# Kernel optimization log

Measured on AMD Instinct MI355X. Metric: run time of the kernel, lower is better.

The kernel has to match this reference:

```python
import jax, jax.numpy as jnp
import numpy as np

H, T, D = 16, 4096, 64   # heads, total packed tokens, head_dim
NSEQ = 8                 # packed variable-length sequences

def setup_inputs() -> dict:
    key = jax.random.key(0)
    k1, k2, k3 = jax.random.split(key, 3)
    q = jax.random.normal(k1, (1, H, T, D), dtype=jnp.float32)
    k = jax.random.normal(k2, (1, H, T, D), dtype=jnp.float32)
    v = jax.random.normal(k3, (1, H, T, D), dtype=jnp.float32)
    # cu_seqlens: prefix sums of per-sequence lengths (equal 512-token segments here)
    cu_seqlens = jnp.arange(NSEQ + 1, dtype=jnp.int32) * (T // NSEQ)
    return {"q": q, "k": k, "v": v, "cu_seqlens": cu_seqlens,
            "block_q_len": 128, "block_k_len": 512}

def reference(q, k, v, cu_seqlens, block_q_len, block_k_len):
    # Faithful to source: scale = 1.0 / d**(-0.5) == sqrt(d)
    d = q.shape[-1]
    scale = 1.0 / d ** (-0.5)
    # [1,H,T,D] -> [T,H,D] packed layout (transpose(1,2).squeeze(0))
    qp = jnp.swapaxes(q, 1, 2)[0]
    kp = jnp.swapaxes(k, 1, 2)[0]
    vp = jnp.swapaxes(v, 1, 2)[0]
    t = qp.shape[0]
    # segment id of each packed token from cu_seqlens
    seg = jnp.searchsorted(cu_seqlens[1:], jnp.arange(t), side="right")
    # tokens attend only within their own sequence (causal=False, dropout=0)
    mask = seg[:, None] == seg[None, :]                      # [T,T]
    scores = jnp.einsum("qhd,khd->hqk", qp, kp) * scale      # [H,T,T]
    scores = jnp.where(mask[None, :, :], scores, -jnp.inf)
    p = jax.nn.softmax(scores, axis=-1)
    out = jnp.einsum("hqk,khd->qhd", p, vp)                  # [T,H,D]
    return out
```

## Files before the change

kernel.cpp:

```cpp
#include <hip/hip_runtime.h>
#include <stdint.h>

typedef float  f32x4  __attribute__((ext_vector_type(4)));
typedef short  bf16x8 __attribute__((ext_vector_type(8)));
typedef unsigned short u16;
typedef u16    u16x4  __attribute__((ext_vector_type(4)));

#define HD 16
#define DD 64
#define BQ 64
#define BK 64

__device__ __forceinline__ u16 f2bf(float f) {
  uint32_t u = __float_as_uint(f);
  u = (u + 0x7FFFu + ((u >> 16) & 1u)) >> 16;
  return (u16)u;
}

__device__ __forceinline__ bf16x8 ldsw8(const u16* base, int row, int col) {
  int idx = (row * 64 + col) ^ ((row & 7) << 3);
  return *reinterpret_cast<const bf16x8*>(base + idx);
}

__global__ __launch_bounds__(256) void fa_fwd(
    const float* __restrict__ q, const float* __restrict__ k,
    const float* __restrict__ v, const int* __restrict__ cu,
    float* __restrict__ out, int T, int nseq)
{
  __shared__ __align__(16) u16 sKhi[BK * DD];
  __shared__ __align__(16) u16 sKlo[BK * DD];
  __shared__ __align__(16) u16 sVt [DD * BK];
  __shared__ __align__(16) u16 sP  [4][16 * BK];

  const int tile = blockIdx.x;
  const int h    = blockIdx.y;

  int seg = -1, row0 = 0, sbeg = 0, send = 0;
  {
    int acc = 0;
    for (int s = 0; s < nseq; ++s) {
      int b = cu[s], e = cu[s + 1];
      int nt = (e - b + BQ - 1) >> 6;
      if (seg < 0 && tile < acc + nt) {
        seg = s;
        int local = tile - acc;
        row0 = b + local * BQ; sbeg = b; send = e;
      }
      acc += nt;
    }
  }
  if (seg < 0) return;
  const int rows = min(BQ, send - row0);

  const int tid  = threadIdx.x;
  const int wv   = tid >> 6;
  const int lane = tid & 63;
  const int g    = lane >> 4;
  const int c    = lane & 15;

  const float SC = 8.0f * 1.4426950408889634f;
  bf16x8 qhi[2], qlo[2];
  {
    const int  qrl = wv * 16 + c;
    const bool qok = qrl < rows;
    const float* qp = q + ((size_t)h * T + (row0 + qrl)) * DD;
    for (int w = 0; w < 2; ++w) {
      int d0 = w * 32 + g * 8;
      float f[8];
      if (qok) {
        float4 a = *reinterpret_cast<const float4*>(qp + d0);
        float4 b = *reinterpret_cast<const float4*>(qp + d0 + 4);
        f[0]=a.x; f[1]=a.y; f[2]=a.z; f[3]=a.w;
        f[4]=b.x; f[5]=b.y; f[6]=b.z; f[7]=b.w;
      } else {
        for (int i = 0; i < 8; ++i) f[i] = 0.f;
      }
      for (int i = 0; i < 8; ++i) {
        float s  = f[i] * SC;
        u16   hb = f2bf(s);
        float hf = __uint_as_float(((uint32_t)hb) << 16);
        u16   lb = f2bf(s - hf);
        qhi[w][i] = (short)hb;
        qlo[w][i] = (short)lb;
      }
    }
  }

  f32x4 zero4 = {0.f, 0.f, 0.f, 0.f};
  f32x4 oacc[4];
  for (int dt = 0; dt < 4; ++dt) oacc[dt] = zero4;
  float mrun[4], lrun[4];
  for (int j = 0; j < 4; ++j) { mrun[j] = -1e30f; lrun[j] = 0.f; }

  for (int kt0 = sbeg; kt0 < send; kt0 += BK) {
    for (int p = 0; p < 4; ++p) {
      int key = p * 16 + (tid >> 4);
      int d0  = (tid & 15) * 4;
      int gk  = kt0 + key;
      float4 kv = {0,0,0,0}, vv = {0,0,0,0};
      if (gk < send) {
        kv = *reinterpret_cast<const float4*>(k + ((size_t)h * T + gk) * DD + d0);
        vv = *reinterpret_cast<const float4*>(v + ((size_t)h * T + gk) * DD + d0);
      }
      float kf[4] = {kv.x, kv.y, kv.z, kv.w};
      u16x4 hi4, lo4;
      for (int i = 0; i < 4; ++i) {
        u16   hb = f2bf(kf[i]);
        float hf = __uint_as_float(((uint32_t)hb) << 16);
        hi4[i] = hb;
        lo4[i] = f2bf(kf[i] - hf);
      }
      int kidx = (key * 64 + d0) ^ ((key & 7) << 3);
      *reinterpret_cast<u16x4*>(sKhi + kidx) = hi4;
      *reinterpret_cast<u16x4*>(sKlo + kidx) = lo4;
      float vf[4] = {vv.x, vv.y, vv.z, vv.w};
      for (int i = 0; i < 4; ++i) {
        int d = d0 + i;
        sVt[(d * 64 + key) ^ ((d & 7) << 3)] = f2bf(vf[i]);
      }
    }
    __syncthreads();

    f32x4 sacc[4];
    for (int kt = 0; kt < 4; ++kt) sacc[kt] = zero4;
    for (int kt = 0; kt < 4; ++kt) {
      int krow = kt * 16 + c;
      bf16x8 kh0 = ldsw8(sKhi, krow,      g * 8);
      bf16x8 kh1 = ldsw8(sKhi, krow, 32 + g * 8);
      bf16x8 kl0 = ldsw8(sKlo, krow,      g * 8);
      bf16x8 kl1 = ldsw8(sKlo, krow, 32 + g * 8);
      sacc[kt] = __builtin_amdgcn_mfma_f32_16x16x32_bf16(qhi[0], kh0, sacc[kt], 0, 0, 0);
      sacc[kt] = __builtin_amdgcn_mfma_f32_16x16x32_bf16(qhi[1], kh1, sacc[kt], 0, 0, 0);
      sacc[kt] = __builtin_amdgcn_mfma_f32_16x16x32_bf16(qlo[0], kh0, sacc[kt], 0, 0, 0);
      sacc[kt] = __builtin_amdgcn_mfma_f32_16x16x32_bf16(qlo[1], kh1, sacc[kt], 0, 0, 0);
      sacc[kt] = __builtin_amdgcn_mfma_f32_16x16x32_bf16(qhi[0], kl0, sacc[kt], 0, 0, 0);
      sacc[kt] = __builtin_amdgcn_mfma_f32_16x16x32_bf16(qhi[1], kl1, sacc[kt], 0, 0, 0);
    }

    if (kt0 + BK > send) {
      for (int kt = 0; kt < 4; ++kt) {
        int gk = kt0 + kt * 16 + c;
        if (gk >= send) {
          sacc[kt][0] = -3.0e38f; sacc[kt][1] = -3.0e38f;
          sacc[kt][2] = -3.0e38f; sacc[kt][3] = -3.0e38f;
        }
      }
    }

    float mrow[4];
    for (int j = 0; j < 4; ++j)
      mrow[j] = fmaxf(fmaxf(sacc[0][j], sacc[1][j]), fmaxf(sacc[2][j], sacc[3][j]));
    for (int off = 1; off < 16; off <<= 1)
      for (int j = 0; j < 4; ++j)
        mrow[j] = fmaxf(mrow[j], __shfl_xor(mrow[j], off, 64));

    float alpha[4];
    for (int j = 0; j < 4; ++j) {
      float mn = fmaxf(mrun[j], mrow[j]);
      alpha[j] = exp2f(mrun[j] - mn);
      mrun[j] = mn;
    }

    float lrow[4] = {0.f, 0.f, 0.f, 0.f};
    u16* pb = sP[wv];
    for (int kt = 0; kt < 4; ++kt) {
      int key = kt * 16 + c;
      for (int j = 0; j < 4; ++j) {
        float pv = exp2f(sacc[kt][j] - mrun[j]);
        lrow[j] += pv;
        int row = g * 4 + j;
        pb[(row * 64 + key) ^ ((row & 7) << 3)] = f2bf(pv);
      }
    }
    for (int off = 1; off < 16; off <<= 1)
      for (int j = 0; j < 4; ++j)
        lrow[j] += __shfl_xor(lrow[j], off, 64);
    for (int j = 0; j < 4; ++j) lrun[j] = lrun[j] * alpha[j] + lrow[j];
    for (int dt = 0; dt < 4; ++dt)
      for (int j = 0; j < 4; ++j) oacc[dt][j] *= alpha[j];

    __syncthreads();

    bf16x8 pf0 = ldsw8(pb, c,      g * 8);
    bf16x8 pf1 = ldsw8(pb, c, 32 + g * 8);
    for (int dt = 0; dt < 4; ++dt) {
      bf16x8 v0 = ldsw8(sVt, dt * 16 + c,      g * 8);
      bf16x8 v1 = ldsw8(sVt, dt * 16 + c, 32 + g * 8);
      oacc[dt] = __builtin_amdgcn_mfma_f32_16x16x32_bf16(pf0, v0, oacc[dt], 0, 0, 0);
      oacc[dt] = __builtin_amdgcn_mfma_f32_16x16x32_bf16(pf1, v1, oacc[dt], 0, 0, 0);
    }
    __syncthreads();
  }

  float inv[4];
  for (int j = 0; j < 4; ++j) inv[j] = 1.0f / lrun[j];
  for (int dt = 0; dt < 4; ++dt) {
    for (int j = 0; j < 4; ++j) {
      int rl = wv * 16 + g * 4 + j;
      if (rl < rows)
        out[((size_t)(row0 + rl) * HD + h) * DD + dt * 16 + c] = oacc[dt][j] * inv[j];
    }
  }
}

extern "C" void kernel_launch(void* const* d_in, const int* in_sizes, int n_in,
                              void* d_out, int out_size, void* d_ws, size_t ws_size,
                              hipStream_t stream) {
  const float* q  = (const float*)d_in[0];
  const float* k  = (const float*)d_in[1];
  const float* v  = (const float*)d_in[2];
  const int*   cu = (const int*)d_in[3];
  int nseq = in_sizes[3] - 1;
  int T    = in_sizes[0] / (HD * DD);
  int nqt  = T / BQ + nseq;
  dim3 grid(nqt, HD);
  fa_fwd<<<grid, dim3(256), 0, stream>>>(q, k, v, cu, (float*)d_out, T, nseq);
}
```

Measured before the change: 155.5 us.

## Prefetch next K/V tile into registers and overlap conversion with compute

New measurement: 267.1 us. 1.72x slower.

```diff
diff --git a/kernel.cpp b/kernel.cpp
--- a/kernel.cpp
+++ b/kernel.cpp
@@ -1,8 +1,8 @@
 #include <hip/hip_runtime.h>
 #include <stdint.h>
 
+typedef short  bf16x8 __attribute__((ext_vector_type(8)));
 typedef float  f32x4  __attribute__((ext_vector_type(4)));
-typedef short  bf16x8 __attribute__((ext_vector_type(8)));
 typedef unsigned short u16;
 typedef u16    u16x4  __attribute__((ext_vector_type(4)));
 
@@ -21,19 +21,27 @@
   int idx = (row * 64 + col) ^ ((row & 7) << 3);
   return *reinterpret_cast<const bf16x8*>(base + idx);
 }
-
-__global__ __launch_bounds__(256) void fa_fwd(
+__device__ __forceinline__ bf16x8 ldsv8(const u16* base, int d, int col) {
+  int idx = (d * 64 + col) ^ ((((d >> 2) ^ d) & 7) << 3);
+  return *reinterpret_cast<const bf16x8*>(base + idx);
+}
+
+__global__ __launch_bounds__(256, 4) void fa_fwd(
     const float* __restrict__ q, const float* __restrict__ k,
     const float* __restrict__ v, const int* __restrict__ cu,
-    float* __restrict__ out, int T, int nseq)
+    float* __restrict__ out, int T, int nseq, int nqt)
 {
   __shared__ __align__(16) u16 sKhi[BK * DD];
   __shared__ __align__(16) u16 sKlo[BK * DD];
   __shared__ __align__(16) u16 sVt [DD * BK];
   __shared__ __align__(16) u16 sP  [4][16 * BK];
 
-  const int tile = blockIdx.x;
-  const int h    = blockIdx.y;
+  const int nwg = nqt * HD;
+  const int x8 = blockIdx.x & 7, mm = blockIdx.x >> 3;
+  const int q8 = nwg >> 3, r8 = nwg & 7;
+  const int wid = (x8 < r8 ? x8 * (q8 + 1) : r8 * (q8 + 1) + (x8 - r8) * q8) + mm;
+  const int h    = wid / nqt;
+  const int tile = wid - h * nqt;
 
   int seg = -1, row0 = 0, sbeg = 0, send = 0;
   {
@@ -61,68 +69,118 @@
   const float SC = 8.0f * 1.4426950408889634f;
   bf16x8 qhi[2], qlo[2];
   {
-    const int  qrl = wv * 16 + c;
-    const bool qok = qrl < rows;
+    const int qrl = min(wv * 16 + c, rows - 1);
     const float* qp = q + ((size_t)h * T + (row0 + qrl)) * DD;
+    #pragma unroll
     for (int w = 0; w < 2; ++w) {
       int d0 = w * 32 + g * 8;
-      float f[8];
-      if (qok) {
-        float4 a = *reinterpret_cast<const float4*>(qp + d0);
-        float4 b = *reinterpret_cast<const float4*>(qp + d0 + 4);
-        f[0]=a.x; f[1]=a.y; f[2]=a.z; f[3]=a.w;
-        f[4]=b.x; f[5]=b.y; f[6]=b.z; f[7]=b.w;
-      } else {
-        for (int i = 0; i < 8; ++i) f[i] = 0.f;
-      }
+      float4 a = *reinterpret_cast<const float4*>(qp + d0);
+      float4 b = *reinterpret_cast<const float4*>(qp + d0 + 4);
+      float f[8] = {a.x, a.y, a.z, a.w, b.x, b.y, b.z, b.w};
+      #pragma unroll
       for (int i = 0; i < 8; ++i) {
         float s  = f[i] * SC;
         u16   hb = f2bf(s);
         float hf = __uint_as_float(((uint32_t)hb) << 16);
-        u16   lb = f2bf(s - hf);
         qhi[w][i] = (short)hb;
-        qlo[w][i] = (short)lb;
-      }
-    }
-  }
+        qlo[w][i] = (short)f2bf(s - hf);
+      }
+    }
+  }
+
+  const int kd0  = (tid & 15) * 4;
+  const int kkey = tid >> 4;
+  const int vdg  = tid & 15;
+  const int vkb  = tid >> 4;
+
+  float4 kraw[4], vrawA[2], vrawB[2];
+  u16x4  khi[4], klo[4];
+  uint32_t vpk[2][4];
+
+  auto issue_loads = [&](int kt0) {
+    #pragma unroll
+    for (int p = 0; p < 4; ++p) {
+      int gk = kt0 + p * 16 + kkey; gk = gk < send ? gk : send - 1;
+      kraw[p] = *reinterpret_cast<const float4*>(k + ((size_t)h * T + gk) * DD + kd0);
+    }
+    #pragma unroll
+    for (int it = 0; it < 2; ++it) {
+      int kp = it * 16 + vkb;
+      int g0 = kt0 + 2 * kp;     g0 = g0 < send ? g0 : send - 1;
+      int g1 = kt0 + 2 * kp + 1; g1 = g1 < send ? g1 : send - 1;
+      vrawA[it] = *reinterpret_cast<const float4*>(v + ((size_t)h * T + g0) * DD + 4 * vdg);
+      vrawB[it] = *reinterpret_cast<const float4*>(v + ((size_t)h * T + g1) * DD + 4 * vdg);
+    }
+  };
+  auto convert_k = [&]() {
+    #pragma unroll
+    for (int p = 0; p < 4; ++p) {
+      float f[4] = {kraw[p].x, kraw[p].y, kraw[p].z, kraw[p].w};
+      #pragma unroll
+      for (int i = 0; i < 4; ++i) {
+        u16   hb = f2bf(f[i]);
+        float hf = __uint_as_float(((uint32_t)hb) << 16);
+        khi[p][i] = hb;
+        klo[p][i] = f2bf(f[i] - hf);
+      }
+    }
+  };
+  auto convert_v = [&]() {
+    #pragma unroll
+    for (int it = 0; it < 2; ++it) {
+      float a[4] = {vrawA[it].x, vrawA[it].y, vrawA[it].z, vrawA[it].w};
+      float b[4] = {vrawB[it].x, vrawB[it].y, vrawB[it].z, vrawB[it].w};
+      #pragma unroll
+      for (int i = 0; i < 4; ++i)
+        vpk[it][i] = (uint32_t)f2bf(a[i]) | ((uint32_t)f2bf(b[i]) << 16);
+    }
+  };
+  auto write_lds = [&]() {
+    #pragma unroll
+    for (int p = 0; p < 4; ++p) {
+      int key = p * 16 + kkey;
+      int idx = (key * 64 + kd0) ^ ((key & 7) << 3);
+      *reinterpret_cast<u16x4*>(sKhi + idx) = khi[p];
+      *reinterpret_cast<u16x4*>(sKlo + idx) = klo[p];
+    }
+    #pragma unroll
+    for (int it = 0; it < 2; ++it) {
+      int kp = it * 16 + vkb;
+      #pragma unroll
+      for (int i = 0; i < 4; ++i) {
+        int d   = 4 * vdg + i;
+        int idx = (d * 64 + 2 * kp) ^ ((((d >> 2) ^ d) & 7) << 3);
+        *reinterpret_cast<uint32_t*>(sVt + idx) = vpk[it][i];
+      }
+    }
+  };
 
   f32x4 zero4 = {0.f, 0.f, 0.f, 0.f};
   f32x4 oacc[4];
+  #pragma unroll
   for (int dt = 0; dt < 4; ++dt) oacc[dt] = zero4;
   float mrun[4], lrun[4];
+  #pragma unroll
   for (int j = 0; j < 4; ++j) { mrun[j] = -1e30f; lrun[j] = 0.f; }
 
-  for (int kt0 = sbeg; kt0 < send; kt0 += BK) {
-    for (int p = 0; p < 4; ++p) {
-      int key = p * 16 + (tid >> 4);
-      int d0  = (tid & 15) * 4;
-      int gk  = kt0 + key;
-      float4 kv = {0,0,0,0}, vv = {0,0,0,0};
-      if (gk < send) {
-        kv = *reinterpret_cast<const float4*>(k + ((size_t)h * T + gk) * DD + d0);
-        vv = *reinterpret_cast<const float4*>(v + ((size_t)h * T + gk) * DD + d0);
-      }
-      float kf[4] = {kv.x, kv.y, kv.z, kv.w};
-      u16x4 hi4, lo4;
-      for (int i = 0; i < 4; ++i) {
-        u16   hb = f2bf(kf[i]);
-        float hf = __uint_as_float(((uint32_t)hb) << 16);
-        hi4[i] = hb;
-        lo4[i] = f2bf(kf[i] - hf);
-      }
-      int kidx = (key * 64 + d0) ^ ((key & 7) << 3);
-      *reinterpret_cast<u16x4*>(sKhi + kidx) = hi4;
-      *reinterpret_cast<u16x4*>(sKlo + kidx) = lo4;
-      float vf[4] = {vv.x, vv.y, vv.z, vv.w};
-      for (int i = 0; i < 4; ++i) {
-        int d = d0 + i;
-        sVt[(d * 64 + key) ^ ((d & 7) << 3)] = f2bf(vf[i]);
-      }
-    }
+  const int nt = (send - sbeg + BK - 1) >> 6;
+
+  issue_loads(sbeg);
+  convert_k();
+  convert_v();
+
+  for (int t = 0; t < nt; ++t) {
+    const int kt0 = sbeg + t * BK;
     __syncthreads();
+    write_lds();
+    __syncthreads();
+    const bool pre = (t + 1 < nt);
+    if (pre) issue_loads(kt0 + BK);
 
     f32x4 sacc[4];
+    #pragma unroll
     for (int kt = 0; kt < 4; ++kt) sacc[kt] = zero4;
+    #pragma unroll
     for (int kt = 0; kt < 4; ++kt) {
       int krow = kt * 16 + c;
       bf16x8 kh0 = ldsw8(sKhi, krow,      g * 8);
@@ -138,6 +196,7 @@
     }
 
     if (kt0 + BK > send) {
+      #pragma unroll
       for (int kt = 0; kt < 4; ++kt) {
         int gk = kt0 + kt * 16 + c;
         if (gk >= send) {
@@ -148,13 +207,17 @@
     }
 
     float mrow[4];
+    #pragma unroll
     for (int j = 0; j < 4; ++j)
       mrow[j] = fmaxf(fmaxf(sacc[0][j], sacc[1][j]), fmaxf(sacc[2][j], sacc[3][j]));
+    #pragma unroll
     for (int off = 1; off < 16; off <<= 1)
+      #pragma unroll
       for (int j = 0; j < 4; ++j)
         mrow[j] = fmaxf(mrow[j], __shfl_xor(mrow[j], off, 64));
 
     float alpha[4];
+    #pragma unroll
     for (int j = 0; j < 4; ++j) {
       float mn = fmaxf(mrun[j], mrow[j]);
       alpha[j] = exp2f(mrun[j] - mn);
@@ -163,8 +226,10 @@
 
     float lrow[4] = {0.f, 0.f, 0.f, 0.f};
     u16* pb = sP[wv];
+    #pragma unroll
     for (int kt = 0; kt < 4; ++kt) {
       int key = kt * 16 + c;
+      #pragma unroll
       for (int j = 0; j < 4; ++j) {
         float pv = exp2f(sacc[kt][j] - mrun[j]);
         lrow[j] += pv;
@@ -172,29 +237,39 @@
         pb[(row * 64 + key) ^ ((row & 7) << 3)] = f2bf(pv);
       }
     }
+    #pragma unroll
     for (int off = 1; off < 16; off <<= 1)
+      #pragma unroll
       for (int j = 0; j < 4; ++j)
         lrow[j] += __shfl_xor(lrow[j], off, 64);
+    #pragma unroll
     for (int j = 0; j < 4; ++j) lrun[j] = lrun[j] * alpha[j] + lrow[j];
+    #pragma unroll
     for (int dt = 0; dt < 4; ++dt)
+      #pragma unroll
       for (int j = 0; j < 4; ++j) oacc[dt][j] *= alpha[j];
 
-    __syncthreads();
+    if (pre) convert_k();
 
     bf16x8 pf0 = ldsw8(pb, c,      g * 8);
     bf16x8 pf1 = ldsw8(pb, c, 32 + g * 8);
+    #pragma unroll
     for (int dt = 0; dt < 4; ++dt) {
-      bf16x8 v0 = ldsw8(sVt, dt * 16 + c,      g * 8);
-      bf16x8 v1 = ldsw8(sVt, dt * 16 + c, 32 + g * 8);
+      bf16x8 v0 = ldsv8(sVt, dt * 16 + c,      g * 8);
+      bf16x8 v1 = ldsv8(sVt, dt * 16 + c, 32 + g * 8);
       oacc[dt] = __builtin_amdgcn_mfma_f32_16x16x32_bf16(pf0, v0, oacc[dt], 0, 0, 0);
       oacc[dt] = __builtin_amdgcn_mfma_f32_16x16x32_bf16(pf1, v1, oacc[dt], 0, 0, 0);
     }
-    __syncthreads();
+
+    if (pre) convert_v();
   }
 
   float inv[4];
+  #pragma unroll
   for (int j = 0; j < 4; ++j) inv[j] = 1.0f / lrun[j];
+  #pragma unroll
   for (int dt = 0; dt < 4; ++dt) {
+    #pragma unroll
     for (int j = 0; j < 4; ++j) {
       int rl = wv * 16 + g * 4 + j;
       if (rl < rows)
@@ -213,6 +288,6 @@
   int nseq = in_sizes[3] - 1;
   int T    = in_sizes[0] / (HD * DD);
   int nqt  = T / BQ + nseq;
-  dim3 grid(nqt, HD);
-  fa_fwd<<<grid, dim3(256), 0, stream>>>(q, k, v, cu, (float*)d_out, T, nseq);
-}
+  int nwg  = nqt * HD;
+  fa_fwd<<<dim3(nwg), dim3(256), 0, stream>>>(q, k, v, cu, (float*)d_out, T, nseq, nqt);
+}
```
